# Kernel optimization log

Hardware: AMD Instinct MI355X
Metric: run time of the kernel (lower is better)

## Reference

```python
import jax, jax.numpy as jnp
import numpy as np

N_HEADS, N_LEVELS, N_POINTS = 8, 4, 4
D_MODEL, D_FFN = 256, 2048
NQ, BS = 900, 4
SPATIAL = np.array([[128, 128], [64, 64], [32, 32], [16, 16]], dtype=np.int64)
HW = int((SPATIAL[:, 0] * SPATIAL[:, 1]).sum())


def _ln(x, g, b):
    mu = x.mean(-1, keepdims=True)
    var = x.var(-1, keepdims=True)
    return (x - mu) / jnp.sqrt(var + 1e-5) * g + b


def _lin(x, w, b):
    return x @ w.T + b


def _msdeform_attn(query, refp, mem, ss, starts, so_w, so_b, aw_w, aw_b, vp_w, vp_b, op_w, op_b):
    # query: (bs, nq, d), refp: (bs, nq, L, 2) in [0,1], mem: (bs, hw, d)
    bs, nq, d = query.shape
    hd = d // N_HEADS
    value = _lin(mem, vp_w, vp_b).reshape(bs, -1, N_HEADS, hd)  # (bs, hw, H, hd)
    offsets = _lin(query, so_w, so_b).reshape(bs, nq, N_HEADS, N_LEVELS, N_POINTS, 2)
    aw = _lin(query, aw_w, aw_b).reshape(bs, nq, N_HEADS, N_LEVELS * N_POINTS)
    aw = jax.nn.softmax(aw, axis=-1).reshape(bs, nq, N_HEADS, N_LEVELS, N_POINTS)
    # offset normalizer is (W, H) per level
    normalizer = jnp.asarray(ss[:, ::-1].copy(), dtype=query.dtype)  # (L, 2)
    loc = refp[:, :, None, :, None, :] + offsets / normalizer[None, None, None, :, None, :]
    out = jnp.zeros((bs, nq, N_HEADS, hd), dtype=query.dtype)
    for l in range(N_LEVELS):
        h_l, w_l = int(ss[l, 0]), int(ss[l, 1])
        vl = value[:, starts[l]:starts[l] + h_l * w_l]  # (bs, h*w, H, hd)
        # grid_sample align_corners=False: pixel coord = loc*size - 0.5
        x = loc[:, :, :, l, :, 0] * w_l - 0.5  # (bs, nq, H, P)
        y = loc[:, :, :, l, :, 1] * h_l - 0.5
        x0 = jnp.floor(x)
        y0 = jnp.floor(y)
        fx = x - x0
        fy = y - y0

        def gather(ix, iy, wgt):
            valid = (ix >= 0) & (ix < w_l) & (iy >= 0) & (iy < h_l)
            idx = (jnp.clip(iy, 0, h_l - 1) * w_l + jnp.clip(ix, 0, w_l - 1)).astype(jnp.int32)
            # (bs, nq, H, P) -> (bs, nq*P, H) to match vl's (bs, hw, H, hd)
            idxt = idx.transpose(0, 1, 3, 2).reshape(bs, nq * N_POINTS, N_HEADS)
            g = jnp.take_along_axis(vl, idxt[..., None], axis=1)  # (bs, nq*P, H, hd)
            g = g.reshape(bs, nq, N_POINTS, N_HEADS, hd).transpose(0, 1, 3, 2, 4)
            return g * (wgt * valid)[..., None]

        x0i = x0.astype(jnp.int32)
        y0i = y0.astype(jnp.int32)
        sampled = (gather(x0i, y0i, (1 - fx) * (1 - fy))
                   + gather(x0i + 1, y0i, fx * (1 - fy))
                   + gather(x0i, y0i + 1, (1 - fx) * fy)
                   + gather(x0i + 1, y0i + 1, fx * fy))  # (bs, nq, H, P, hd)
        out = out + (sampled * aw[:, :, :, l, :, None]).sum(axis=3)
    return _lin(out.reshape(bs, nq, d), op_w, op_b)


def _fwd(tgt, query_pos, memory, ref_points,
         sa_in_w, sa_in_b, sa_out_w, sa_out_b,
         ln1_g, ln1_b, ln2_g, ln2_b, ln3_g, ln3_b,
         so_w, so_b, aw_w, aw_b, vp_w, vp_b, op_w, op_b,
         ff1_w, ff1_b, ff2_w, ff2_b, spatial_shapes, level_start_index):
    nq, bs, d = tgt.shape
    hd = d // N_HEADS
    ss = np.asarray(spatial_shapes)
    starts = np.asarray(level_start_index)
    # ---- self attention (q = k = tgt + pos, v = tgt) ----
    qk = tgt + query_pos
    q = _lin(qk, sa_in_w[:d], sa_in_b[:d]).reshape(nq, bs, N_HEADS, hd)
    k = _lin(qk, sa_in_w[d:2 * d], sa_in_b[d:2 * d]).reshape(nq, bs, N_HEADS, hd)
    v = _lin(tgt, sa_in_w[2 * d:], sa_in_b[2 * d:]).reshape(nq, bs, N_HEADS, hd)
    scores = jnp.einsum('qbhd,kbhd->bhqk', q, k) / np.sqrt(hd).astype(tgt.dtype)
    attn = jax.nn.softmax(scores, axis=-1)
    sa = jnp.einsum('bhqk,kbhd->qbhd', attn, v).reshape(nq, bs, d)
    sa = _lin(sa, sa_out_w, sa_out_b)
    tgt = _ln(tgt + sa, ln2_g, ln2_b)
    # ---- deformable cross attention ----
    ca = _msdeform_attn((tgt + query_pos).transpose(1, 0, 2),
                        ref_points.transpose(1, 0, 2, 3),
                        memory.transpose(1, 0, 2), ss, starts,
                        so_w, so_b, aw_w, aw_b, vp_w, vp_b, op_w, op_b)
    tgt = _ln(tgt + ca.transpose(1, 0, 2), ln1_g, ln1_b)
    # ---- FFN ----
    ff = _lin(jax.nn.relu(_lin(tgt, ff1_w, ff1_b)), ff2_w, ff2_b)
    return _ln(tgt + ff, ln3_g, ln3_b)


def setup_inputs() -> dict:
    key = jax.random.key(0)
    ks = iter(jax.random.split(key, 32))
    d, dffn = D_MODEL, D_FFN
    nofs = N_HEADS * N_LEVELS * N_POINTS
    w = lambda *s: jax.random.normal(next(ks), s, dtype=jnp.float32) * 0.02
    starts = np.concatenate([[0], np.cumsum(SPATIAL[:, 0] * SPATIAL[:, 1])[:-1]]).astype(np.int64)
    return {
        'tgt': jax.random.normal(next(ks), (NQ, BS, d), dtype=jnp.float32),
        'query_pos': jax.random.normal(next(ks), (NQ, BS, d), dtype=jnp.float32),
        'memory': jax.random.normal(next(ks), (HW, BS, d), dtype=jnp.float32),
        'ref_points': jax.random.uniform(next(ks), (NQ, BS, N_LEVELS, 2), dtype=jnp.float32),
        'sa_in_w': w(3 * d, d), 'sa_in_b': w(3 * d), 'sa_out_w': w(d, d), 'sa_out_b': w(d),
        'ln1_g': jnp.ones((d,)), 'ln1_b': jnp.zeros((d,)),
        'ln2_g': jnp.ones((d,)), 'ln2_b': jnp.zeros((d,)),
        'ln3_g': jnp.ones((d,)), 'ln3_b': jnp.zeros((d,)),
        'so_w': w(nofs * 2, d), 'so_b': jax.random.normal(next(ks), (nofs * 2,), dtype=jnp.float32) * 0.5,
        'aw_w': w(nofs, d), 'aw_b': w(nofs),
        'vp_w': w(d, d), 'vp_b': w(d), 'op_w': w(d, d), 'op_b': w(d),
        'ff1_w': w(dffn, d), 'ff1_b': w(dffn), 'ff2_w': w(d, dffn), 'ff2_b': w(d),
        'spatial_shapes': SPATIAL, 'level_start_index': starts,
    }


def reference(tgt, query_pos, memory, ref_points, sa_in_w, sa_in_b, sa_out_w, sa_out_b, ln1_g, ln1_b, ln2_g, ln2_b, ln3_g, ln3_b, so_w, so_b, aw_w, aw_b, vp_w, vp_b, op_w, op_b, ff1_w, ff1_b, ff2_w, ff2_b, spatial_shapes, level_start_index):
    return _fwd(tgt, query_pos, memory, ref_points, sa_in_w, sa_in_b, sa_out_w, sa_out_b,
                ln1_g, ln1_b, ln2_g, ln2_b, ln3_g, ln3_b, so_w, so_b, aw_w, aw_b,
                vp_w, vp_b, op_w, op_b, ff1_w, ff1_b, ff2_w, ff2_b,
                spatial_shapes, level_start_index)
```

## Files before the change

### kernel.cpp

```cpp
#include <hip/hip_runtime.h>
#include <hip/hip_bf16.h>

#define D_MODEL 256
#define N_HEADS 8
#define HD 32
#define NQ 900
#define BS 4
#define MROWS (NQ * BS)
#define HW_TOT 21760
#define VROWS (HW_TOT * BS)

typedef __attribute__((ext_vector_type(8))) short bf16x8;
typedef __attribute__((ext_vector_type(4))) float f32x4;

__device__ inline short f2b(float f) {
  union { __hip_bfloat16 h; short s; } u;
  u.h = __float2bfloat16(f);
  return u.s;
}
__device__ inline float bu2f(unsigned short u) {
  union { unsigned int i; float f; } c;
  c.i = ((unsigned int)u) << 16;
  return c.f;
}
__device__ inline bf16x8 bzero8() {
  bf16x8 v;
#pragma unroll
  for (int j = 0; j < 8; ++j) v[j] = 0;
  return v;
}
__device__ inline f32x4 fzero4() {
  f32x4 v;
#pragma unroll
  for (int j = 0; j < 4; ++j) v[j] = 0.f;
  return v;
}

#define GLL16(gsrc, ldst)                                                     \
  __builtin_amdgcn_global_load_lds(                                           \
      (__attribute__((address_space(1))) void*)(gsrc),                        \
      (__attribute__((address_space(3))) void*)(ldst), 16, 0, 0)

__global__ __launch_bounds__(256) void prep_all(const float* __restrict__ s0,
                                                const float* __restrict__ s1,
                                                const float* __restrict__ s2,
                                                const float* __restrict__ s3,
                                                const float* __restrict__ s4,
                                                const float* __restrict__ s5,
                                                const float* __restrict__ s6,
                                                const float* __restrict__ s7,
                                                short* __restrict__ dst,
                                                const float* __restrict__ tgt,
                                                const float* __restrict__ qpos,
                                                short* __restrict__ tgtb,
                                                short* __restrict__ qkb,
                                                const float* __restrict__ so_b,
                                                const float* __restrict__ aw_b,
                                                float* __restrict__ biasSOAW) {
  int i = blockIdx.x * 256 + threadIdx.x;
  if (i < 1540096) {
    const float* s; int off;
    if (i < 196608)      { s = s0; off = 0; }
    else if (i < 262144) { s = s1; off = 196608; }
    else if (i < 327680) { s = s2; off = 262144; }
    else if (i < 360448) { s = s3; off = 327680; }
    else if (i < 425984) { s = s4; off = 360448; }
    else if (i < 491520) { s = s5; off = 425984; }
    else if (i < 1015808){ s = s6; off = 491520; }
    else                 { s = s7; off = 1015808; }
    dst[i] = f2b(s[i - off]);
  } else {
    int j = i - 1540096;
    float t = tgt[j], p = qpos[j];
    tgtb[j] = f2b(t);
    qkb[j] = f2b(t + p);
    if (j < 384) biasSOAW[j] = (j < 256) ? so_b[j] : aw_b[j - 256];
  }
}

template <int BN, int AF32, int OUTF32, int RELU>
__device__ __forceinline__ void gemm_core(const void* __restrict__ Xv,
                                          const short* __restrict__ W,
                                          const float* __restrict__ bias,
                                          void* __restrict__ outv,
                                          int M, int N, int K, int m0, int n0,
                                          int t0, int t1, int addBias,
                                          short* __restrict__ smem) {
  constexpr int NF = BN / 16;
  short* sA = smem;
  short* sB = smem + 2 * 2048;
  const int tid = threadIdx.x;
  const int wave = tid >> 6, lane = tid & 63;
  const int l15 = lane & 15, l4 = lane >> 4;
  const int wr = wave * 16;
  const float* Xf = (const float*)Xv;
  const short* Xh = (const short*)Xv;

  f32x4 acc[NF];
#pragma unroll
  for (int f = 0; f < NF; ++f) acc[f] = fzero4();

  const int alr = wave * 16 + (lane >> 2);
  const int ags = (lane & 3) ^ ((alr >> 1) & 3);
  const int arow = tid >> 2, ak = tid & 3;
  const int agsrc = ak ^ ((arow >> 1) & 3);
  float4 ra0, ra1;

  auto stageB = [&](int t, int buf) {
    short* bb = sB + buf * BN * 32;
#pragma unroll
    for (int j = 0; j < BN / 64; ++j) {
      int lr = j * 64 + alr;
      int gs = (lane & 3) ^ ((lr >> 1) & 3);
      const short* src = W + (size_t)(n0 + lr) * K + t * 32 + gs * 8;
      GLL16(src, bb + (j * 64 + wave * 16) * 32);
    }
  };
  auto stageA_gll = [&](int t, int buf) {
    const short* src = Xh + (size_t)(m0 + alr) * K + t * 32 + ags * 8;
    GLL16(src, sA + buf * 2048 + wave * 512);
  };
  auto loadA_f32 = [&](int t) {
    const float* p = Xf + (size_t)(m0 + arow) * K + t * 32 + agsrc * 8;
    ra0 = *reinterpret_cast<const float4*>(p);
    ra1 = *reinterpret_cast<const float4*>(p + 4);
  };
  auto writeA_f32 = [&](int buf) {
    bf16x8 v;
    v[0] = f2b(ra0.x); v[1] = f2b(ra0.y); v[2] = f2b(ra0.z); v[3] = f2b(ra0.w);
    v[4] = f2b(ra1.x); v[5] = f2b(ra1.y); v[6] = f2b(ra1.z); v[7] = f2b(ra1.w);
    *reinterpret_cast<bf16x8*>(&sA[buf * 2048 + arow * 32 + ak * 8]) = v;
  };
  auto compute = [&](int buf) {
    const int r = wr + l15;
    bf16x8 av = *reinterpret_cast<const bf16x8*>(
        &sA[buf * 2048 + r * 32 + ((l4 ^ ((r >> 1) & 3)) * 8)]);
#pragma unroll
    for (int f = 0; f < NF; ++f) {
      const int rb = f * 16 + l15;
      bf16x8 bv = *reinterpret_cast<const bf16x8*>(
          &sB[buf * BN * 32 + rb * 32 + ((l4 ^ ((rb >> 1) & 3)) * 8)]);
      acc[f] = __builtin_amdgcn_mfma_f32_16x16x32_bf16(av, bv, acc[f], 0, 0, 0);
    }
  };

  if constexpr (AF32) { loadA_f32(t0); writeA_f32(0); }
  else stageA_gll(t0, 0);
  stageB(t0, 0);
  __syncthreads();

  int buf = 0;
  for (int t = t0; t < t1; ++t) {
    if (t + 1 < t1) {
      if constexpr (AF32) loadA_f32(t + 1);
      else stageA_gll(t + 1, buf ^ 1);
      stageB(t + 1, buf ^ 1);
    }
    compute(buf);
    if (AF32 && t + 1 < t1) writeA_f32(buf ^ 1);
    __syncthreads();
    buf ^= 1;
  }

#pragma unroll
  for (int f = 0; f < NF; ++f) {
    int col = n0 + f * 16 + l15;
    float bfv = addBias ? bias[col] : 0.f;
#pragma unroll
    for (int i = 0; i < 4; ++i) {
      int row = m0 + wr + l4 * 4 + i;
      if (row >= M) continue;
      float v = acc[f][i] + bfv;
      if (RELU) v = fmaxf(v, 0.f);
      if constexpr (OUTF32)
        ((float*)outv)[(size_t)row * N + col] = v;
      else
        ((short*)outv)[(size_t)row * N + col] = f2b(v);
    }
  }
}

template <int BN, int AF32, int OUTF32, int RELU>
__global__ __launch_bounds__(256) void gemm2(const void* __restrict__ Xv,
                                             const short* __restrict__ W,
                                             const float* __restrict__ bias,
                                             void* __restrict__ outv,
                                             int M, int N, int K) {
  __shared__ __align__(16) short smem[2 * 2048 + 2 * BN * 32];
  gemm_core<BN, AF32, OUTF32, RELU>(Xv, W, bias, outv, M, N, K,
                                    blockIdx.x * 64, blockIdx.y * BN,
                                    0, K / 32, 1, smem);
}

__global__ __launch_bounds__(256) void gemm_splitk(const void* __restrict__ Xv,
                                                   const short* __restrict__ W,
                                                   const float* __restrict__ bias,
                                                   float* __restrict__ outp,
                                                   int M, int N, int K) {
  __shared__ __align__(16) short smem[2 * 2048 + 2 * 64 * 32];
  const int kc = blockIdx.z;
  const int ntc = K / 32 / 4;
  gemm_core<64, 0, 1, 0>(Xv, W, bias, outp + (size_t)kc * M * N, M, N, K,
                         blockIdx.x * 64, blockIdx.y * 64,
                         kc * ntc, (kc + 1) * ntc, kc == 0, smem);
}

__global__ __launch_bounds__(256) void qkv_gemm(const short* __restrict__ qkb,
                                                const short* __restrict__ tgtb,
                                                const short* __restrict__ Wqkv,
                                                const float* __restrict__ sa_in_b,
                                                short* __restrict__ QKb,
                                                short* __restrict__ Vb) {
  __shared__ __align__(16) short smem[2 * 2048 + 2 * 64 * 32];
  int bx = blockIdx.x;
  if (bx < 456) {
    gemm_core<64, 0, 0, 0>(qkb, Wqkv, sa_in_b, QKb, MROWS, 512, 256,
                           (bx % 57) * 64, (bx / 57) * 64, 0, 8, 1, smem);
  } else {
    bx -= 456;
    gemm_core<64, 0, 0, 0>(tgtb, Wqkv + 512 * 256, sa_in_b + 512, Vb, MROWS, 256, 256,
                           (bx % 57) * 64, (bx / 57) * 64, 0, 8, 1, smem);
  }
}

__device__ __forceinline__ void flash_body(const short* __restrict__ QK,
                                           const short* __restrict__ V,
                                           short* __restrict__ O,
                                           int bid, short* __restrict__ smem) {
  const int bh = bid & 31, b = bh >> 3, h = bh & 7;
  const int q0 = (bid >> 5) * 64;
  const int tid = threadIdx.x, wave = tid >> 6, lane = tid & 63;
  const int l15 = lane & 15, l4 = lane >> 4;
  const int cb = h * 32;

  short* sQ = smem;
  short* sK = smem + 2048;
  short* sVt = smem + 6144;
  short* sP = smem + 10752;

  const int sr = wave * 16 + (lane >> 2);
  const int sgs = (lane & 3) ^ (sr & 3);

  auto stageK = [&](int kt, int buf) {
    const short* src = QK + (size_t)((kt * 64 + sr) * 4 + b) * 512 + 256 + cb + sgs * 8;
    GLL16(src, sK + buf * 2048 + wave * 512);
  };
  const int vrow = tid >> 2, vdof = (tid & 3) * 8;
  const int vkp = vrow ^ (((vdof >> 3) & 3) << 4);
  auto loadV = [&](int kt) -> bf16x8 {
    int kk = kt * 64 + vrow;
    return (kk < NQ)
        ? *reinterpret_cast<const bf16x8*>(V + (size_t)(kk * 4 + b) * 256 + cb + vdof)
        : bzero8();
  };
  auto writeV = [&](bf16x8 vv, int buf) {
    short* dst = sVt + buf * 2304;
#pragma unroll
    for (int j = 0; j < 8; ++j) dst[(vdof + j) * 72 + vkp] = vv[j];
  };

  {
    const short* qsrc = QK + (size_t)((q0 + sr) * 4 + b) * 512 + cb + sgs * 8;
    GLL16(qsrc, sQ + wave * 512);
  }
  stageK(0, 0);
  {
    bf16x8 v0 = loadV(0);
    writeV(v0, 0);
  }
  __syncthreads();

  const int wr = wave * 16;
  const int rq = wr + l15;
  const bf16x8 aq = *reinterpret_cast<const bf16x8*>(&sQ[rq * 32 + ((l4 ^ (rq & 3)) * 8)]);

  float mrow[4], lrow[4];
#pragma unroll
  for (int i = 0; i < 4; ++i) { mrow[i] = -1e30f; lrow[i] = 0.f; }
  f32x4 accO[2];
  accO[0] = fzero4(); accO[1] = fzero4();

  const int pswz = (((wr >> 2) + l4) & 3) << 3;
  const int pswzr = (((wr >> 2) + (l15 >> 2)) & 3) << 3;

  for (int kt = 0; kt < 15; ++kt) {
    const int k0 = kt * 64;
    const int buf = kt & 1;
    const bool more = (kt + 1 < 15);
    bf16x8 vnext = bzero8();
    if (more) {
      stageK(kt + 1, buf ^ 1);
      vnext = loadV(kt + 1);
    }

    f32x4 s[4];
#pragma unroll
    for (int f = 0; f < 4; ++f) {
      const int rb = f * 16 + l15;
      bf16x8 bk = *reinterpret_cast<bf16x8*>(
          &sK[buf * 2048 + rb * 32 + ((l4 ^ (rb & 3)) * 8)]);
      s[f] = __builtin_amdgcn_mfma_f32_16x16x32_bf16(aq, bk, fzero4(), 0, 0, 0);
    }
#pragma unroll
    for (int f = 0; f < 4; ++f) {
      bool valid = (k0 + f * 16 + l15) < NQ;
#pragma unroll
      for (int i = 0; i < 4; ++i) {
        float sv = s[f][i] * 0.17677669529663687f;
        s[f][i] = valid ? sv : -1e30f;
      }
    }
    float mx[4];
#pragma unroll
    for (int i = 0; i < 4; ++i)
      mx[i] = fmaxf(fmaxf(s[0][i], s[1][i]), fmaxf(s[2][i], s[3][i]));
#pragma unroll
    for (int off = 1; off < 16; off <<= 1)
#pragma unroll
      for (int i = 0; i < 4; ++i) mx[i] = fmaxf(mx[i], __shfl_xor(mx[i], off));

    float alpha[4], rs[4];
#pragma unroll
    for (int i = 0; i < 4; ++i) {
      float mn = fmaxf(mrow[i], mx[i]);
      alpha[i] = __expf(mrow[i] - mn);
      mrow[i] = mn;
      rs[i] = 0.f;
    }
#pragma unroll
    for (int f = 0; f < 4; ++f)
#pragma unroll
      for (int i = 0; i < 4; ++i) {
        float p = __expf(s[f][i] - mrow[i]);
        rs[i] += p;
        sP[(wr + l4 * 4 + i) * 72 + ((f * 16 + l15) ^ pswz)] = f2b(p);
      }
#pragma unroll
    for (int off = 1; off < 16; off <<= 1)
#pragma unroll
      for (int i = 0; i < 4; ++i) rs[i] += __shfl_xor(rs[i], off);
#pragma unroll
    for (int i = 0; i < 4; ++i) lrow[i] = lrow[i] * alpha[i] + rs[i];
#pragma unroll
    for (int nf = 0; nf < 2; ++nf)
#pragma unroll
      for (int i = 0; i < 4; ++i) accO[nf][i] *= alpha[i];

#pragma unroll
    for (int ks = 0; ks < 2; ++ks) {
      bf16x8 ap = *reinterpret_cast<bf16x8*>(
          &sP[(wr + l15) * 72 + ((ks * 32 + l4 * 8) ^ pswzr)]);
#pragma unroll
      for (int nf = 0; nf < 2; ++nf) {
        const int d = nf * 16 + l15;
        const int kb = (ks * 32 + l4 * 8) ^ (((d >> 3) & 3) << 4);
        bf16x8 bv = *reinterpret_cast<bf16x8*>(&sVt[buf * 2304 + d * 72 + kb]);
        accO[nf] = __builtin_amdgcn_mfma_f32_16x16x32_bf16(ap, bv, accO[nf], 0, 0, 0);
      }
    }
    if (more) writeV(vnext, buf ^ 1);
    __syncthreads();
  }

#pragma unroll
  for (int nf = 0; nf < 2; ++nf)
#pragma unroll
    for (int i = 0; i < 4; ++i) {
      int q = q0 + wr + l4 * 4 + i;
      if (q < NQ)
        O[(size_t)(q * 4 + b) * 256 + cb + nf * 16 + l15] = f2b(accO[nf][i] / lrow[i]);
    }
}

__device__ __forceinline__ void value_core(const float* __restrict__ memory,
                                           const short* __restrict__ W,
                                           const float* __restrict__ vp_b,
                                           short* __restrict__ value, int vb,
                                           short* __restrict__ smem) {
  float* sAf = (float*)smem;
  short* sB = smem + 8192;
  const int tid = threadIdx.x;
  const int wave = tid >> 6, lane = tid & 63;
  const int l15 = lane & 15, l4 = lane >> 4;
  const int wr = wave * 16;
  const int m0 = (vb >> 1) * 64;
  const int n0 = (vb & 1) * 128;

  const int ar0 = wave * 16 + (lane >> 3);
  const int ag = (lane & 7) ^ (lane >> 3);
  auto stageA = [&](int t, int buf) {
    const float* s0 = memory + (size_t)(m0 + ar0) * 256 + t * 32 + ag * 4;
    GLL16(s0, (short*)sAf + buf * 4096 + wave * 1024);
    const float* s1 = memory + (size_t)(m0 + ar0 + 8) * 256 + t * 32 + ag * 4;
    GLL16(s1, (short*)sAf + buf * 4096 + wave * 1024 + 512);
  };
  const int blr = wave * 16 + (lane >> 2);
  auto stageB = [&](int t, int buf) {
#pragma unroll
    for (int j = 0; j < 2; ++j) {
      int lr = j * 64 + blr;
      int gs = (lane & 3) ^ ((lr >> 1) & 3);
      const short* src = W + (size_t)(n0 + lr) * 256 + t * 32 + gs * 8;
      GLL16(src, sB + buf * 4096 + (j * 64 + wave * 16) * 32);
    }
  };

  f32x4 acc[8];
#pragma unroll
  for (int f = 0; f < 8; ++f) acc[f] = fzero4();

  auto compute = [&](int buf) {
    const int r = wr + l15;
    const int rx = r & 7;
    const float* ap = sAf + buf * 2048 + r * 32;
    float4 a0 = *reinterpret_cast<const float4*>(ap + (((2 * l4) ^ rx) * 4));
    float4 a1 = *reinterpret_cast<const float4*>(ap + (((2 * l4 + 1) ^ rx) * 4));
    bf16x8 av;
    av[0] = f2b(a0.x); av[1] = f2b(a0.y); av[2] = f2b(a0.z); av[3] = f2b(a0.w);
    av[4] = f2b(a1.x); av[5] = f2b(a1.y); av[6] = f2b(a1.z); av[7] = f2b(a1.w);
#pragma unroll
    for (int f = 0; f < 8; ++f) {
      const int rb = f * 16 + l15;
      bf16x8 bv = *reinterpret_cast<const bf16x8*>(
          &sB[buf * 4096 + rb * 32 + ((l4 ^ ((rb >> 1) & 3)) * 8)]);
      acc[f] = __builtin_amdgcn_mfma_f32_16x16x32_bf16(av, bv, acc[f], 0, 0, 0);
    }
  };

  stageA(0, 0);
  stageB(0, 0);
  __syncthreads();
  int buf = 0;
  for (int t = 0; t < 8; ++t) {
    if (t + 1 < 8) {
      stageA(t + 1, buf ^ 1);
      stageB(t + 1, buf ^ 1);
    }
    compute(buf);
    __syncthreads();
    buf ^= 1;
  }

#pragma unroll
  for (int f = 0; f < 8; ++f) {
    const int col = n0 + f * 16 + l15;
    const float bb = vp_b[col];
#pragma unroll
    for (int i = 0; i < 4; ++i)
      value[(size_t)(m0 + wr + l4 * 4 + i) * 256 + col] = f2b(acc[f][i] + bb);
  }
}

__global__ __launch_bounds__(256) void flash_value(const short* __restrict__ QKb,
                                                   const short* __restrict__ Vb,
                                                   short* __restrict__ Ob,
                                                   const float* __restrict__ memory,
                                                   const short* __restrict__ Wvp,
                                                   const float* __restrict__ vp_b,
                                                   short* __restrict__ value) {
  __shared__ __align__(16) short smem[16384];
  int bx = blockIdx.x;
  if (bx < 480) {
    flash_body(QKb, Vb, Ob, bx, smem);
  } else {
    value_core(memory, Wvp, vp_b, value, bx - 480, smem);
  }
}

__global__ __launch_bounds__(256) void ln_kernel(const float* __restrict__ A,
                                                 const float* __restrict__ B,
                                                 const float* __restrict__ g,
                                                 const float* __restrict__ bb,
                                                 float* __restrict__ outF,
                                                 short* __restrict__ outB,
                                                 const float* __restrict__ addv) {
  const int row = blockIdx.x;
  const int t = threadIdx.x;
  const size_t base = (size_t)row * D_MODEL;
  float x = A[base + t] + B[base + t];
  float s = x, s2 = x * x;
#pragma unroll
  for (int off = 32; off; off >>= 1) {
    s += __shfl_xor(s, off);
    s2 += __shfl_xor(s2, off);
  }
  __shared__ float wsum[4], wsum2[4];
  const int w = t >> 6;
  if ((t & 63) == 0) { wsum[w] = s; wsum2[w] = s2; }
  __syncthreads();
  s = wsum[0] + wsum[1] + wsum[2] + wsum[3];
  s2 = wsum2[0] + wsum2[1] + wsum2[2] + wsum2[3];
  const float mu = s * (1.f / 256.f);
  const float var = s2 * (1.f / 256.f) - mu * mu;
  const float inv = rsqrtf(var + 1e-5f);
  float y = (x - mu) * inv * g[t] + bb[t];
  outF[base + t] = y;
  if (outB) outB[base + t] = f2b(y + (addv ? addv[base + t] : 0.f));
}

__global__ __launch_bounds__(256) void ln4_kernel(const float* __restrict__ A,
                                                  const float* __restrict__ P,
                                                  const float* __restrict__ g,
                                                  const float* __restrict__ bb,
                                                  float* __restrict__ outF) {
  const int row = blockIdx.x;
  const int t = threadIdx.x;
  const size_t base = (size_t)row * D_MODEL + t;
  const size_t stride = (size_t)MROWS * D_MODEL;
  float x = A[base] + P[base] + P[base + stride] + P[base + 2 * stride] + P[base + 3 * stride];
  float s = x, s2 = x * x;
#pragma unroll
  for (int off = 32; off; off >>= 1) {
    s += __shfl_xor(s, off);
    s2 += __shfl_xor(s2, off);
  }
  __shared__ float wsum[4], wsum2[4];
  const int w = t >> 6;
  if ((t & 63) == 0) { wsum[w] = s; wsum2[w] = s2; }
  __syncthreads();
  s = wsum[0] + wsum[1] + wsum[2] + wsum[3];
  s2 = wsum2[0] + wsum2[1] + wsum2[2] + wsum2[3];
  const float mu = s * (1.f / 256.f);
  const float var = s2 * (1.f / 256.f) - mu * mu;
  const float inv = rsqrtf(var + 1e-5f);
  outF[base] = (x - mu) * inv * g[t] + bb[t];
}

__global__ __launch_bounds__(256) void msds_kernel(const unsigned short* __restrict__ value,
                                                   const float* __restrict__ soaw,
                                                   const float* __restrict__ refp,
                                                   unsigned short* __restrict__ out) {
  const int tid = threadIdx.x;
  const int row = blockIdx.x * 8 + (tid >> 5);
  const int lane32 = tid & 31;
  const int h = lane32 >> 2;
  const int dp = (lane32 & 3) * 8;
  const int b = row & 3;

  const int WL[4] = {128, 64, 32, 16};
  const int ST[4] = {0, 16384, 20480, 21504};

  const float* awp = soaw + (size_t)row * 384 + 256 + h * 16;
  float awv[16];
  float m = -1e30f;
#pragma unroll
  for (int i = 0; i < 16; ++i) { awv[i] = awp[i]; m = fmaxf(m, awv[i]); }
  float s = 0.f;
#pragma unroll
  for (int i = 0; i < 16; ++i) { awv[i] = __expf(awv[i] - m); s += awv[i]; }
  const float invs = 1.f / s;

  const float* offp = soaw + (size_t)row * 384 + h * 32;
  float acc[8];
#pragma unroll
  for (int j = 0; j < 8; ++j) acc[j] = 0.f;

#pragma unroll
  for (int l = 0; l < 4; ++l) {
    const int wl = WL[l], hl = WL[l], st = ST[l];
    const float rx = refp[((size_t)row * 4 + l) * 2 + 0];
    const float ry = refp[((size_t)row * 4 + l) * 2 + 1];
#pragma unroll
    for (int p = 0; p < 4; ++p) {
      const float ox = offp[l * 8 + p * 2 + 0];
      const float oy = offp[l * 8 + p * 2 + 1];
      const float x = (rx + ox / (float)wl) * (float)wl - 0.5f;
      const float y = (ry + oy / (float)hl) * (float)hl - 0.5f;
      const float x0f = floorf(x), y0f = floorf(y);
      const int x0 = (int)x0f, y0 = (int)y0f;
      const float fx = x - x0f, fy = y - y0f;
      const float a = awv[l * 4 + p] * invs;
      const float w00 = (1.f - fx) * (1.f - fy);
      const float w10 = fx * (1.f - fy);
      const float w01 = (1.f - fx) * fy;
      const float w11 = fx * fy;
      float sv[8];
#pragma unroll
      for (int j = 0; j < 8; ++j) sv[j] = 0.f;
      auto gat = [&](int ix, int iy, float wgt) {
        if (ix >= 0 && ix < wl && iy >= 0 && iy < hl) {
          const unsigned short* p2 =
              value + ((size_t)((st + iy * wl + ix) * 4 + b)) * 256 + h * 32 + dp;
          bf16x8 u = *reinterpret_cast<const bf16x8*>(p2);
#pragma unroll
          for (int j = 0; j < 8; ++j) sv[j] += wgt * bu2f((unsigned short)u[j]);
        }
      };
      gat(x0, y0, w00);
      gat(x0 + 1, y0, w10);
      gat(x0, y0 + 1, w01);
      gat(x0 + 1, y0 + 1, w11);
#pragma unroll
      for (int j = 0; j < 8; ++j) acc[j] += a * sv[j];
    }
  }
  bf16x8 o;
#pragma unroll
  for (int j = 0; j < 8; ++j) o[j] = f2b(acc[j]);
  *reinterpret_cast<bf16x8*>(&out[(size_t)row * 256 + h * 32 + dp]) = o;
}

extern "C" void kernel_launch(void* const* d_in, const int* in_sizes, int n_in,
                              void* d_out, int out_size, void* d_ws, size_t ws_size,
                              hipStream_t stream) {
  const float* tgt      = (const float*)d_in[0];
  const float* qpos     = (const float*)d_in[1];
  const float* memory   = (const float*)d_in[2];
  const float* refp     = (const float*)d_in[3];
  const float* sa_in_w  = (const float*)d_in[4];
  const float* sa_in_b  = (const float*)d_in[5];
  const float* sa_out_w = (const float*)d_in[6];
  const float* sa_out_b = (const float*)d_in[7];
  const float* ln1_g = (const float*)d_in[8];
  const float* ln1_b = (const float*)d_in[9];
  const float* ln2_g = (const float*)d_in[10];
  const float* ln2_b = (const float*)d_in[11];
  const float* ln3_g = (const float*)d_in[12];
  const float* ln3_b = (const float*)d_in[13];
  const float* so_w = (const float*)d_in[14];
  const float* so_b = (const float*)d_in[15];
  const float* aw_w = (const float*)d_in[16];
  const float* aw_b = (const float*)d_in[17];
  const float* vp_w = (const float*)d_in[18];
  const float* vp_b = (const float*)d_in[19];
  const float* op_w = (const float*)d_in[20];
  const float* op_b = (const float*)d_in[21];
  const float* ff1_w = (const float*)d_in[22];
  const float* ff1_b = (const float*)d_in[23];
  const float* ff2_w = (const float*)d_in[24];
  const float* ff2_b = (const float*)d_in[25];

  float* out = (float*)d_out;
  float* ws = (float*)d_ws;

  short* Wb       = (short*)ws;
  float* biasSOAW = ws + 770048;
  short* tgtb   = (short*)(ws + 770432);
  short* qkb    = (short*)(ws + 1231232);
  short* QKb    = (short*)(ws + 1692032);
  short* Vb     = (short*)(ws + 2613632);
  short* Ob     = (short*)(ws + 3074432);
  float* SA     = ws + 3535232;
  float* F      = ws + 4456832;
  short* qk2b   = (short*)(ws + 5378432);
  float* SOAW   = ws + 5839232;
  short* value  = (short*)(ws + 7221632);
  short* sampled= (short*)(ws + 18362752);
  float* CA     = ws + 18823552;
  float* tgt3   = ws + 19745152;
  short* tgt3b  = (short*)(ws + 20666752);
  short* H      = (short*)(ws + 21127552);
  float* FFp    = ws + 7221632;

  const short* Wqkv = Wb;
  const short* Wsa  = Wb + 196608;
  const short* Wso  = Wb + 262144;
  const short* Wvp  = Wb + 360448;
  const short* Wop  = Wb + 425984;
  const short* Wff1 = Wb + 491520;
  const short* Wff2 = Wb + 1015808;

  prep_all<<<9616, 256, 0, stream>>>(sa_in_w, sa_out_w, so_w, aw_w, vp_w, op_w,
                                     ff1_w, ff2_w, Wb, tgt, qpos, tgtb, qkb,
                                     so_b, aw_b, biasSOAW);
  qkv_gemm<<<684, 256, 0, stream>>>(qkb, tgtb, Wqkv, sa_in_b, QKb, Vb);
  flash_value<<<3200, 256, 0, stream>>>(QKb, Vb, Ob, memory, Wvp, vp_b, value);
  gemm2<64, 0, 1, 0><<<dim3(57, 4), 256, 0, stream>>>(Ob, Wsa, sa_out_b, SA, MROWS, 256, 256);
  ln_kernel<<<MROWS, 256, 0, stream>>>(tgt, SA, ln2_g, ln2_b, F, qk2b, qpos);
  gemm2<64, 0, 1, 0><<<dim3(57, 6), 256, 0, stream>>>(qk2b, Wso, biasSOAW, SOAW, MROWS, 384, 256);
  msds_kernel<<<450, 256, 0, stream>>>((const unsigned short*)value, SOAW, refp,
                                       (unsigned short*)sampled);
  gemm2<64, 0, 1, 0><<<dim3(57, 4), 256, 0, stream>>>(sampled, Wop, op_b, CA, MROWS, 256, 256);
  ln_kernel<<<MROWS, 256, 0, stream>>>(F, CA, ln1_g, ln1_b, tgt3, tgt3b, nullptr);
  gemm2<64, 0, 0, 1><<<dim3(57, 32), 256, 0, stream>>>(tgt3b, Wff1, ff1_b, H, MROWS, 2048, 256);
  gemm_splitk<<<dim3(57, 4, 4), 256, 0, stream>>>(H, Wff2, ff2_b, FFp, MROWS, 256, 2048);
  ln4_kernel<<<MROWS, 256, 0, stream>>>(tgt3, FFp, ln3_g, ln3_b, out);
}
```

Baseline: 162.8 us.

## Prefetch two stages ahead in value projection and remap block tile order

```diff
diff --git a/kernel.cpp b/kernel.cpp
--- a/kernel.cpp
+++ b/kernel.cpp
@@ -383,8 +383,8 @@
   const int wave = tid >> 6, lane = tid & 63;
   const int l15 = lane & 15, l4 = lane >> 4;
   const int wr = wave * 16;
-  const int m0 = (vb >> 1) * 64;
-  const int n0 = (vb & 1) * 128;
+  const int m0 = (((vb >> 4) << 3) | (vb & 7)) * 64;
+  const int n0 = ((vb >> 3) & 1) * 128;
 
   const int ar0 = wave * 16 + (lane >> 3);
   const int ag = (lane & 7) ^ (lane >> 3);
@@ -427,18 +427,29 @@
     }
   };
 
-  stageA(0, 0);
-  stageB(0, 0);
-  __syncthreads();
-  int buf = 0;
+  stageA(0, 0); stageB(0, 0);
+  stageA(1, 1); stageB(1, 1);
+  asm volatile("s_waitcnt vmcnt(4)" ::: "memory");
+  __builtin_amdgcn_sched_barrier(0);
+  __builtin_amdgcn_s_barrier();
+  __builtin_amdgcn_sched_barrier(0);
+
+#pragma unroll
   for (int t = 0; t < 8; ++t) {
+    const int buf = t & 1;
+    compute(buf);
+    asm volatile("s_waitcnt lgkmcnt(0)" ::: "memory");
+    __builtin_amdgcn_sched_barrier(0);
+    __builtin_amdgcn_s_barrier();
+    __builtin_amdgcn_sched_barrier(0);
+    if (t + 2 < 8) { stageA(t + 2, buf); stageB(t + 2, buf); }
     if (t + 1 < 8) {
-      stageA(t + 1, buf ^ 1);
-      stageB(t + 1, buf ^ 1);
-    }
-    compute(buf);
-    __syncthreads();
-    buf ^= 1;
+      if (t + 2 < 8) asm volatile("s_waitcnt vmcnt(4)" ::: "memory");
+      else           asm volatile("s_waitcnt vmcnt(0)" ::: "memory");
+      __builtin_amdgcn_sched_barrier(0);
+      __builtin_amdgcn_s_barrier();
+      __builtin_amdgcn_sched_barrier(0);
+    }
   }
 
 #pragma unroll
```

Measured after the change: 161.4 us. Within noise of the previous version (-0.8%).
